# Performance work log

Measured on AMD Instinct MI355X. Metric: run time of the kernel, lower is better.

Reference implementation:

```python
import jax, jax.numpy as jnp
import numpy as np

BINS = 32
C_Z = 128
B, L = 2, 768
NUM_CLASSES = 2 * BINS + 2  # 66


def setup_inputs() -> dict:
    key = jax.random.key(0)
    k1, k2, k3 = jax.random.split(key, 3)
    residue_index = jnp.sort(jax.random.randint(k1, (B, L), 0, 1024), axis=-1)
    residue_mask = jnp.ones((B, L), dtype=bool)
    W = jax.random.normal(k2, (NUM_CLASSES, C_Z), dtype=jnp.float32)  # linear.weight.T
    b = jax.random.normal(k3, (C_Z,), dtype=jnp.float32)
    return {"residue_index": residue_index, "residue_mask": residue_mask, "W": W, "b": b}


def reference(residue_index, residue_mask, W, b):
    # pairwise relative position, clipped into bins -> class index in [1, 2*BINS+1]
    diff = residue_index[:, None, :] - residue_index[:, :, None]  # [B, L, L]
    idx = jnp.clip(diff, -BINS, BINS) + BINS + 1
    # one_hot(idx) @ W + b  ==  gather rows of W
    z = W[idx] + b  # [B, L, L, C_Z]
    pair_mask = residue_mask[:, :, None] & residue_mask[:, None, :]
    return z * pair_mask[..., None].astype(z.dtype)
```

## Files before the change

### kernel.cpp

```cpp
#include <hip/hip_runtime.h>


constexpr int BINS = 32;
constexpr int CZ   = 128;
constexpr int NC   = 2 * BINS + 2;
constexpr int B_   = 2;
constexpr int L_   = 768;
constexpr int NPAIRS = B_ * L_ * L_;
constexpr int GROUPS_PER_BLOCK = 8;
constexpr int NBLOCKS = 2048;

typedef float vfloat4 __attribute__((ext_vector_type(4)));

__global__ __launch_bounds__(256) void relpos_kernel(
    const int*  __restrict__ residue_index,
    const void* __restrict__ residue_mask,
    const float* __restrict__ W,
    const float* __restrict__ bias,
    float* __restrict__ out)
{
    __shared__ float wb[NC * CZ];
    __shared__ int   ridx[B_ * L_];
    __shared__ float maskf[B_ * L_];

    const int tid = threadIdx.x;

    const unsigned int v0 = *(const unsigned int*)residue_mask;
    const bool byte_layout = (v0 & 0xFFFFFF00u) != 0u;

    const vfloat4* W4  = (const vfloat4*)W;
    const vfloat4* bi4 = (const vfloat4*)bias;
    vfloat4* wb4 = (vfloat4*)wb;
    for (int k = tid; k < NC * CZ / 4; k += 256) {
        vfloat4 w = W4[k];
        w += bi4[k & (CZ / 4 - 1)];
        wb4[k] = w;
    }
    for (int k = tid; k < B_ * L_; k += 256) {
        ridx[k] = residue_index[k];
        int m = byte_layout ? (int)((const unsigned char*)residue_mask)[k]
                            : ((const int*)residue_mask)[k];
        maskf[k] = m ? 1.0f : 0.0f;
    }
    __syncthreads();

    const int group = tid >> 5;
    const int lane  = tid & 31;

    int p = blockIdx.x * GROUPS_PER_BLOCK + group;
    const int pstride = gridDim.x * GROUPS_PER_BLOCK;
    for (; p < NPAIRS; p += pstride) {
        const int b = p / (L_ * L_);
        const int r = p - b * (L_ * L_);
        const int i = r / L_;
        const int j = r - i * L_;
        const int o = b * L_;

        const int diff = ridx[o + j] - ridx[o + i];
        const int idx  = min(max(diff, -BINS), BINS) + BINS + 1;
        const float m  = maskf[o + i] * maskf[o + j];

        vfloat4 v = ((const vfloat4*)(wb + idx * CZ))[lane];
        v *= m;

        __builtin_nontemporal_store(v, (vfloat4*)(out + (size_t)p * CZ) + lane);
    }
}

extern "C" void kernel_launch(void* const* d_in, const int* in_sizes, int n_in,
                              void* d_out, int out_size, void* d_ws, size_t ws_size,
                              hipStream_t stream) {
    const int*  residue_index = (const int*)d_in[0];
    const void* residue_mask  = d_in[1];
    const float* W    = (const float*)d_in[2];
    const float* bias = (const float*)d_in[3];
    float* out = (float*)d_out;

    relpos_kernel<<<NBLOCKS, 256, 0, stream>>>(residue_index, residue_mask, W, bias, out);
}
```

Before: 617.5 us.

## Assign one output row per block and drop per-pair index division

```diff
diff --git a/kernel.cpp b/kernel.cpp
--- a/kernel.cpp
+++ b/kernel.cpp
@@ -6,13 +6,11 @@
 constexpr int NC   = 2 * BINS + 2;
 constexpr int B_   = 2;
 constexpr int L_   = 768;
-constexpr int NPAIRS = B_ * L_ * L_;
-constexpr int GROUPS_PER_BLOCK = 8;
-constexpr int NBLOCKS = 2048;
+constexpr int NROWS = B_ * L_;
 
 typedef float vfloat4 __attribute__((ext_vector_type(4)));
 
-__global__ __launch_bounds__(256) void relpos_kernel(
+__global__ __launch_bounds__(256) void relpos_row_kernel(
     const int*  __restrict__ residue_index,
     const void* __restrict__ residue_mask,
     const float* __restrict__ W,
@@ -20,10 +18,14 @@
     float* __restrict__ out)
 {
     __shared__ float wb[NC * CZ];
-    __shared__ int   ridx[B_ * L_];
-    __shared__ float maskf[B_ * L_];
+    __shared__ int   ridx_row[L_];
+    __shared__ float mask_row[L_];
 
     const int tid = threadIdx.x;
+    const int row = blockIdx.x;
+    const int b   = row / L_;
+    const int i   = row - b * L_;
+    const int o   = b * L_;
 
     const unsigned int v0 = *(const unsigned int*)residue_mask;
     const bool byte_layout = (v0 & 0xFFFFFF00u) != 0u;
@@ -32,38 +34,32 @@
     const vfloat4* bi4 = (const vfloat4*)bias;
     vfloat4* wb4 = (vfloat4*)wb;
     for (int k = tid; k < NC * CZ / 4; k += 256) {
-        vfloat4 w = W4[k];
-        w += bi4[k & (CZ / 4 - 1)];
-        wb4[k] = w;
+        wb4[k] = W4[k] + bi4[k & (CZ / 4 - 1)];
     }
-    for (int k = tid; k < B_ * L_; k += 256) {
-        ridx[k] = residue_index[k];
-        int m = byte_layout ? (int)((const unsigned char*)residue_mask)[k]
-                            : ((const int*)residue_mask)[k];
-        maskf[k] = m ? 1.0f : 0.0f;
+    for (int k = tid; k < L_; k += 256) {
+        ridx_row[k] = residue_index[o + k];
+        int m = byte_layout ? (int)((const unsigned char*)residue_mask)[o + k]
+                            : ((const int*)residue_mask)[o + k];
+        mask_row[k] = m ? 1.0f : 0.0f;
     }
     __syncthreads();
 
+    const int   ri_i = ridx_row[i];
+    const float m_i  = mask_row[i];
+
     const int group = tid >> 5;
     const int lane  = tid & 31;
+    float* rowout = out + (size_t)row * L_ * CZ;
 
-    int p = blockIdx.x * GROUPS_PER_BLOCK + group;
-    const int pstride = gridDim.x * GROUPS_PER_BLOCK;
-    for (; p < NPAIRS; p += pstride) {
-        const int b = p / (L_ * L_);
-        const int r = p - b * (L_ * L_);
-        const int i = r / L_;
-        const int j = r - i * L_;
-        const int o = b * L_;
-
-        const int diff = ridx[o + j] - ridx[o + i];
+    #pragma unroll 4
+    for (int j = group; j < L_; j += 8) {
+        const int diff = ridx_row[j] - ri_i;
         const int idx  = min(max(diff, -BINS), BINS) + BINS + 1;
-        const float m  = maskf[o + i] * maskf[o + j];
+        const float m  = m_i * mask_row[j];
 
         vfloat4 v = ((const vfloat4*)(wb + idx * CZ))[lane];
         v *= m;
-
-        __builtin_nontemporal_store(v, (vfloat4*)(out + (size_t)p * CZ) + lane);
+        ((vfloat4*)(rowout + j * CZ))[lane] = v;
     }
 }
 
@@ -76,5 +72,5 @@
     const float* bias = (const float*)d_in[3];
     float* out = (float*)d_out;
 
-    relpos_kernel<<<NBLOCKS, 256, 0, stream>>>(residue_index, residue_mask, W, bias, out);
+    relpos_row_kernel<<<NROWS, 256, 0, stream>>>(residue_index, residue_mask, W, bias, out);
 }
```

Result: faster. 599.9 us (-2.9%).
